# Kernel tuning notes

Hardware: AMD Instinct MI355X
Metric: run time of the kernel (lower is better)

## Reference

```python
import jax, jax.numpy as jnp
import numpy as np

B, N, C = 16, 65536, 21          # batch, anchors, classes (class 0 = background)
TH_CONF = 0.05                   # confidence threshold
TH_IOU = 0.5                     # NMS IoU threshold
TOP_K = 200                      # candidates kept per (batch, class) before NMS
V0, V1 = 0.1, 0.2                # SSD box-coder variances


def setup_inputs() -> dict:
    key = jax.random.key(0)
    k1, k2, k3, k4 = jax.random.split(key, 4)
    conf = jax.random.normal(k1, (B, N, C), dtype=jnp.float32)
    loc = jax.random.normal(k2, (B, N, 4), dtype=jnp.float32)
    # anchors in center form (cx, cy, w, h), normalized coords
    cxcy = jax.random.uniform(k3, (N, 2), dtype=jnp.float32)
    wh = 0.02 + 0.2 * jax.random.uniform(k4, (N, 2), dtype=jnp.float32)
    anchors = jnp.concatenate([cxcy, wh], axis=-1)
    return {"conf": conf, "loc": loc, "anchors": anchors}


def _decode(anchors, loc):
    # SSD decode: anchors [N,4] center form, loc [B,N,4] offsets -> [B,N,4] xyxy
    a_xy, a_wh = anchors[:, :2], anchors[:, 2:]
    xy = a_xy + loc[..., :2] * V0 * a_wh
    wh = a_wh * jnp.exp(loc[..., 2:] * V1)
    return jnp.concatenate([xy - 0.5 * wh, xy + 0.5 * wh], axis=-1)


def _iou(boxes):
    # boxes [K,4] xyxy -> pairwise IoU [K,K]
    area = jnp.maximum(boxes[:, 2] - boxes[:, 0], 0.0) * jnp.maximum(boxes[:, 3] - boxes[:, 1], 0.0)
    lt = jnp.maximum(boxes[:, None, :2], boxes[None, :, :2])
    rb = jnp.minimum(boxes[:, None, 2:], boxes[None, :, 2:])
    wh = jnp.maximum(rb - lt, 0.0)
    inter = wh[..., 0] * wh[..., 1]
    union = area[:, None] + area[None, :] - inter
    return inter / jnp.maximum(union, 1e-9)


def _nms_keep(iou, valid):
    # greedy NMS over score-sorted candidates; valid = (score >= TH_CONF)
    K = iou.shape[0]
    idx = jnp.arange(K)

    def body(keep, xs):
        row, v, i = xs
        suppressed = jnp.any((row > TH_IOU) & keep & (idx < i))
        k = v & (~suppressed)
        return keep.at[i].set(k), 0

    keep, _ = jax.lax.scan(body, jnp.zeros((K,), dtype=bool), (iou, valid, idx))
    return keep


def reference(conf, loc, anchors):
    score = jax.nn.softmax(conf, axis=2)            # [B,N,C]
    boxes = _decode(anchors, loc)                   # [B,N,4]
    # skip background class 0 (cls_base = 1 for softmax classifier)
    cls_scores = jnp.swapaxes(score[..., 1:], 1, 2)  # [B,C-1,N]
    top_s, top_i = jax.lax.top_k(cls_scores, TOP_K)  # [B,C-1,K], sorted desc
    top_boxes = jax.vmap(lambda bx, ix: bx[ix])(boxes, top_i)  # [B,C-1,K,4]
    valid = top_s >= TH_CONF
    keep = jax.vmap(jax.vmap(lambda b, v: _nms_keep(_iou(b), v)))(top_boxes, valid)  # [B,C-1,K]
    out_boxes = jnp.where(keep[..., None], top_boxes, 0.0)
    out_scores = jnp.where(keep, top_s, 0.0)
    return jnp.concatenate([out_boxes, out_scores[..., None]], axis=-1)  # [B,C-1,K,5]
```

## Files before the change

kernel.cpp:

```cpp
#include <hip/hip_runtime.h>
#include <stdint.h>

#define NB     16
#define NANCH  65536
#define NC     21
#define NCLS   20
#define NCOL   (NB * NCLS)
#define TOPK   200
#define NBINS  1024
#define CAP    256
#define CAPCOL 4096
#define CAPFAST 2048
#define CNTSTRIDE 16

constexpr float TH      = 0.05f;
constexpr float TPRE    = 0.20f;
constexpr float SCALE20 = (float)NBINS / 0.80f;
constexpr float SCALE05 = (float)NBINS / 0.95f;

__device__ __forceinline__ int bin20(float s) {
  int b = (int)((s - 0.20f) * SCALE20);
  return b < 0 ? 0 : (b > NBINS - 1 ? NBINS - 1 : b);
}
__device__ __forceinline__ int bin05(float s) {
  int b = (int)((s - 0.05f) * SCALE05);
  return b < 0 ? 0 : (b > NBINS - 1 ? NBINS - 1 : b);
}

__device__ __forceinline__ unsigned long long rl64(unsigned long long v, int lane) {
  unsigned int lo = __builtin_amdgcn_readlane((int)(unsigned int)v, lane);
  unsigned int hi = __builtin_amdgcn_readlane((int)(unsigned int)(v >> 32), lane);
  return ((unsigned long long)hi << 32) | lo;
}

__device__ __forceinline__ void softmax_tail(const float* x, float* e, float& S) {
  float m = x[0];
#pragma unroll
  for (int c = 1; c < NC; ++c) m = fmaxf(m, x[c]);
#pragma unroll
  for (int c = 0; c < NC; ++c) e[c] = expf(x[c] - m);
  float r0 = e[0] + e[8],  r1 = e[1] + e[9],  r2 = e[2] + e[10], r3 = e[3] + e[11];
  float r4 = e[4] + e[12], r5 = e[5] + e[13], r6 = e[6] + e[14], r7 = e[7] + e[15];
  S = ((r0 + r1) + (r2 + r3)) + ((r4 + r5) + (r6 + r7));
  S += e[16]; S += e[17]; S += e[18]; S += e[19]; S += e[20];
}

__global__ __launch_bounds__(256) void softmax_collect_kernel(
    const float* __restrict__ conf,
    unsigned int* __restrict__ cnt, unsigned long long* __restrict__ cand) {
  const int tid = threadIdx.x;
  __shared__ float ld[256 * NC];
  const float4* src = (const float4*)conf + (long long)blockIdx.x * 1344;
  float4* dst4 = (float4*)ld;
#pragma unroll
  for (int i = 0; i < 5; ++i) dst4[tid + i * 256] = src[tid + i * 256];
  if (tid < 64) dst4[tid + 1280] = src[tid + 1280];
  __syncthreads();

  const int a = blockIdx.x * 256 + tid;
  const int b = a >> 16;
  const int n = a & (NANCH - 1);
  float x[NC];
#pragma unroll
  for (int c = 0; c < NC; ++c) x[c] = ld[tid * NC + c];
  float e[NC], S;
  softmax_tail(x, e, S);
  const float t = TPRE * S;
  unsigned int takemask = 0;
#pragma unroll
  for (int c = 0; c < NCLS; ++c)
    if (e[c + 1] >= t) takemask |= (1u << c);

  __shared__ unsigned int wcnt[4][NCLS];
  __shared__ unsigned int wbase[4][NCLS];
  const int wave = tid >> 6, lane = tid & 63;
#pragma unroll
  for (int c = 0; c < NCLS; ++c) {
    unsigned long long m = __ballot((takemask >> c) & 1);
    if (lane == 0) wcnt[wave][c] = (unsigned int)__popcll(m);
  }
  __syncthreads();
  if (tid < NCLS) {
    const int c = tid;
    unsigned int t0 = wcnt[0][c], t1 = wcnt[1][c], t2 = wcnt[2][c], t3 = wcnt[3][c];
    unsigned int tot = t0 + t1 + t2 + t3;
    unsigned int base = tot ? atomicAdd(&cnt[(b * NCLS + c) * CNTSTRIDE], tot) : 0u;
    wbase[0][c] = base;
    wbase[1][c] = base + t0;
    wbase[2][c] = base + t0 + t1;
    wbase[3][c] = base + t0 + t1 + t2;
  }
  __syncthreads();
#pragma unroll
  for (int c = 0; c < NCLS; ++c) {
    bool take = (takemask >> c) & 1;
    unsigned long long m = __ballot(take);
    if (take) {
      float s = e[c + 1] / S;
      unsigned int off = wbase[wave][c] +
                         (unsigned int)__popcll(m & ((1ULL << lane) - 1));
      if (off < CAPCOL) {
        unsigned int key = __float_as_uint(s) | 0x80000000u;
        cand[(long long)(b * NCLS + c) * CAPCOL + off] =
            ((unsigned long long)(key ^ 0xFFFFFFFFu) << 32) |
            (unsigned long long)(unsigned int)n;
      }
    }
  }
}

__global__ __launch_bounds__(1024) void topk_nms_kernel(
    const unsigned long long* __restrict__ candg,
    const unsigned int* __restrict__ cnt,
    const float* __restrict__ conf, const float* __restrict__ loc,
    const float* __restrict__ anchors, float* __restrict__ out) {
  const int bc = blockIdx.x;
  const int b  = bc / NCLS;
  const int cls = bc % NCLS;
  const int tid = threadIdx.x;
  const int lane = tid & 63;

  __shared__ unsigned int hist[NBINS];
  __shared__ unsigned int part[256];
  __shared__ int s_sel, s_n;
  __shared__ unsigned long long cand[CAP];
  __shared__ float4 box4[TOPK];
  __shared__ float sscore[TOPK];
  __shared__ unsigned long long adj[TOPK][4];
  __shared__ unsigned long long keptw[4];

  int nc = (int)cnt[bc * CNTSTRIDE];
  const bool fast = (nc >= TOPK && nc <= CAPFAST);
  for (int i = tid; i < NBINS; i += 1024) hist[i] = 0;
  if (tid < CAP) cand[tid] = ~0ULL;
  if (tid < TOPK) { box4[tid] = make_float4(0.f,0.f,0.f,0.f); sscore[tid] = 0.f; }
  if (tid == 0) s_n = 0;
  __syncthreads();

  const unsigned long long* cg = candg + (long long)bc * CAPCOL;
  if (fast) {
    for (int i = tid; i < nc; i += 1024) {
      unsigned int key = (unsigned int)(cg[i] >> 32) ^ 0xFFFFFFFFu;
      float s = __uint_as_float(key ^ 0x80000000u);
      atomicAdd(&hist[bin20(s)], 1u);
    }
  } else {
    for (int n = tid; n < NANCH; n += 1024) {
      const float* row = conf + ((long long)b * NANCH + n) * NC;
      float x[NC], e[NC], S;
#pragma unroll
      for (int c = 0; c < NC; ++c) x[c] = row[c];
      softmax_tail(x, e, S);
      float s = e[cls + 1] / S;
      if (s >= TH) atomicAdd(&hist[bin05(s)], 1u);
    }
  }
  __syncthreads();

  if (tid < 256)
    part[tid] = hist[tid*4] + hist[tid*4+1] + hist[tid*4+2] + hist[tid*4+3];
  if (tid == 0) s_sel = -1;
  __syncthreads();
  if (tid < 64) {
    unsigned int p4 = part[tid*4] + part[tid*4+1] + part[tid*4+2] + part[tid*4+3];
    unsigned int sfx = p4;
#pragma unroll
    for (int off = 1; off < 64; off <<= 1) {
      unsigned int o = __shfl_down(sfx, off);
      if (tid + off < 64) sfx += o;
    }
    unsigned int above = sfx - p4;
    if (above < TOPK && sfx >= TOPK) {
      unsigned int cum = above; int sel = tid * 16; bool found = false;
      for (int q = 3; q >= 0 && !found; --q) {
        unsigned int pc = part[tid*4 + q];
        if (cum + pc >= TOPK) {
          for (int i = 3; i >= 0; --i) {
            unsigned int c = hist[(tid*4+q)*4 + i];
            if (cum + c >= TOPK) { sel = (tid*4+q)*4 + i; found = true; break; }
            cum += c;
          }
        } else cum += pc;
      }
      s_sel = sel;
    }
  }
  __syncthreads();
  const int sel = s_sel;

  if (fast) {
    const int ncr = (nc + 1023) & ~1023;
    for (int i = tid; i < ncr; i += 1024) {
      bool have = i < nc;
      unsigned long long k64 = have ? cg[i] : 0ULL;
      bool takeit = false;
      if (have) {
        unsigned int key = (unsigned int)(k64 >> 32) ^ 0xFFFFFFFFu;
        float s = __uint_as_float(key ^ 0x80000000u);
        takeit = bin20(s) >= sel;
      }
      unsigned long long m = __ballot(takeit);
      int cw = (int)__popcll(m);
      int base = 0;
      if (lane == 0 && cw) base = atomicAdd(&s_n, cw);
      base = __shfl(base, 0);
      if (takeit) {
        int pos = base + (int)__popcll(m & ((1ULL << lane) - 1));
        if (pos < CAP) cand[pos] = k64;
      }
    }
  } else {
    for (int n0 = tid; n0 < NANCH; n0 += 1024) {
      const float* row = conf + ((long long)b * NANCH + n0) * NC;
      float x[NC], e[NC], S;
#pragma unroll
      for (int c = 0; c < NC; ++c) x[c] = row[c];
      softmax_tail(x, e, S);
      float s = e[cls + 1] / S;
      bool takeit = (s >= TH && (sel < 0 || bin05(s) >= sel));
      unsigned long long m = __ballot(takeit);
      int cw = (int)__popcll(m);
      int base = 0;
      if (lane == 0 && cw) base = atomicAdd(&s_n, cw);
      base = __shfl(base, 0);
      if (takeit) {
        int pos = base + (int)__popcll(m & ((1ULL << lane) - 1));
        if (pos < CAP) {
          unsigned int key = __float_as_uint(s) | 0x80000000u;
          cand[pos] = ((unsigned long long)(key ^ 0xFFFFFFFFu) << 32) |
                      (unsigned long long)(unsigned int)n0;
        }
      }
    }
  }
  __syncthreads();
  int ncand = s_n; if (ncand > CAP) ncand = CAP;
  const int nsel = (ncand < TOPK) ? ncand : TOPK;

  if (tid < CAP && tid < ncand) {
    const unsigned long long key64 = cand[tid];
    int rank = 0;
#pragma unroll 8
    for (int j = 0; j < CAP; ++j)
      rank += (cand[j] < key64) ? 1 : 0;
    if (rank < TOPK) {
      unsigned int key = (unsigned int)(key64 >> 32) ^ 0xFFFFFFFFu;
      float s = __uint_as_float(key ^ 0x80000000u);
      int idx = (int)(unsigned int)(key64 & 0xFFFFFFFFu);
      float4 anc = ((const float4*)anchors)[idx];
      float4 l   = ((const float4*)loc)[(long long)b * NANCH + idx];
      float cx = anc.x + (l.x * 0.1f) * anc.z;
      float cy = anc.y + (l.y * 0.1f) * anc.w;
      float w  = anc.z * expf(l.z * 0.2f);
      float h  = anc.w * expf(l.w * 0.2f);
      box4[rank] = make_float4(cx - 0.5f * w, cy - 0.5f * h,
                               cx + 0.5f * w, cy + 0.5f * h);
      sscore[rank] = s;
    }
  }
  __syncthreads();

  if (tid < TOPK * 4) {
    const int row = tid >> 2, w = tid & 3;
    const float4 a4 = box4[row];
    const float aar = fmaxf(a4.z - a4.x, 0.f) * fmaxf(a4.w - a4.y, 0.f);
    const int jend = (w < 3) ? 64 : (TOPK - 192);
    unsigned long long roww = 0;
#pragma unroll 4
    for (int jj = 0; jj < jend; ++jj) {
      const int j = (w << 6) + jj;
      float4 b4 = box4[j];
      float jar = fmaxf(b4.z - b4.x, 0.f) * fmaxf(b4.w - b4.y, 0.f);
      float ltx = fmaxf(a4.x, b4.x);
      float lty = fmaxf(a4.y, b4.y);
      float rbx = fminf(a4.z, b4.z);
      float rby = fminf(a4.w, b4.w);
      float iw = fmaxf(rbx - ltx, 0.0f);
      float ih = fmaxf(rby - lty, 0.0f);
      float inter = iw * ih;
      float uni = aar + jar - inter;
      float um = fmaxf(uni, 1e-9f);
      float half = 0.5f * um;
      bool hit;
      if (inter > half * 1.000001f)      hit = true;
      else if (inter < half * 0.999999f) hit = false;
      else                               hit = (inter / um > 0.5f);
      roww |= (unsigned long long)(hit ? 1u : 0u) << jj;
    }
    const int myw = row >> 6, myb = row & 63;
    unsigned long long tri = (w < myw) ? 0ULL
                           : (w > myw) ? ~0ULL
                           : ((myb == 63) ? 0ULL : (~0ULL << (myb + 1)));
    adj[row][w] = roww & tri;
  }
  __syncthreads();

  if (tid < 64) {
    const int l = tid;
    unsigned long long r0[4], r1[4], r2[4], r3[4];
#pragma unroll
    for (int w = 0; w < 4; ++w) {
      r0[w] = adj[l][w];
      r1[w] = adj[l + 64][w];
      r2[w] = adj[l + 128][w];
      r3[w] = (l < 8) ? adj[l + 192][w] : 0ULL;
    }
    unsigned long long sup0 = 0, sup1 = 0, sup2 = 0, sup3 = 0;
    unsigned long long k0 = 0, k1 = 0, k2 = 0, k3 = 0;
#pragma unroll 1
    for (int ii = 0; ii < 64; ++ii) {
      unsigned long long live = ((~sup0 >> ii) & 1ULL) &
                                (unsigned long long)(ii < nsel);
      unsigned long long mask = 0ULL - live;
      k0 |= live << ii;
      sup0 |= rl64(r0[0], ii) & mask; sup1 |= rl64(r0[1], ii) & mask;
      sup2 |= rl64(r0[2], ii) & mask; sup3 |= rl64(r0[3], ii) & mask;
    }
#pragma unroll 1
    for (int ii = 0; ii < 64; ++ii) {
      unsigned long long live = ((~sup1 >> ii) & 1ULL) &
                                (unsigned long long)((64 + ii) < nsel);
      unsigned long long mask = 0ULL - live;
      k1 |= live << ii;
      sup1 |= rl64(r1[1], ii) & mask; sup2 |= rl64(r1[2], ii) & mask;
      sup3 |= rl64(r1[3], ii) & mask;
    }
#pragma unroll 1
    for (int ii = 0; ii < 64; ++ii) {
      unsigned long long live = ((~sup2 >> ii) & 1ULL) &
                                (unsigned long long)((128 + ii) < nsel);
      unsigned long long mask = 0ULL - live;
      k2 |= live << ii;
      sup2 |= rl64(r2[2], ii) & mask; sup3 |= rl64(r2[3], ii) & mask;
    }
#pragma unroll 1
    for (int ii = 0; ii < 8; ++ii) {
      unsigned long long live = ((~sup3 >> ii) & 1ULL) &
                                (unsigned long long)((192 + ii) < nsel);
      unsigned long long mask = 0ULL - live;
      k3 |= live << ii;
      sup3 |= rl64(r3[3], ii) & mask;
    }
    if (l == 0) { keptw[0] = k0; keptw[1] = k1; keptw[2] = k2; keptw[3] = k3; }
  }
  __syncthreads();

  const float* fb = (const float*)box4;
  float* ob = out + (long long)bc * (TOPK * 5);
  for (int pos = tid; pos < TOPK * 5; pos += 1024) {
    int row = pos / 5;
    int k5  = pos - row * 5;
    bool kp = (keptw[row >> 6] >> (row & 63)) & 1ULL;
    float val = (k5 == 4) ? sscore[row] : fb[row * 4 + k5];
    ob[pos] = kp ? val : 0.0f;
  }
}

extern "C" void kernel_launch(void* const* d_in, const int* in_sizes, int n_in,
                              void* d_out, int out_size, void* d_ws, size_t ws_size,
                              hipStream_t stream) {
  const float* conf    = (const float*)d_in[0];
  const float* loc     = (const float*)d_in[1];
  const float* anchors = (const float*)d_in[2];
  float* out = (float*)d_out;

  char* ws = (char*)d_ws;
  unsigned long long* cand = (unsigned long long*)ws;
  unsigned int*       cnt  = (unsigned int*)(ws + 10485760);

  hipMemsetAsync(ws + 10485760, 0, 320 * CNTSTRIDE * 4, stream);
  softmax_collect_kernel<<<(NB * NANCH) / 256, 256, 0, stream>>>(conf, cnt, cand);
  topk_nms_kernel<<<NCOL, 1024, 0, stream>>>(cand, cnt, conf, loc, anchors, out);
}
```

Before: 94.14 us.

## Process two (batch,class) columns per block in top-k NMS kernel

The top-k/NMS kernel now handles two columns per 1024-thread block, so it launches half as many blocks. Histogram, selection, ranking, IoU and greedy-NMS phases run both columns side by side, which raises thread utilisation in the phases that previously used only 64-800 threads. The cost is doubled shared memory per block, which may lower occupancy. With 320 columns the grid drops to 160 blocks, fewer than the number of CUs on the device, so parallelism across CUs falls.

```diff
diff --git a/kernel.cpp b/kernel.cpp
--- a/kernel.cpp
+++ b/kernel.cpp
@@ -114,162 +114,194 @@
     const unsigned int* __restrict__ cnt,
     const float* __restrict__ conf, const float* __restrict__ loc,
     const float* __restrict__ anchors, float* __restrict__ out) {
-  const int bc = blockIdx.x;
-  const int b  = bc / NCLS;
-  const int cls = bc % NCLS;
+  const int bc0 = blockIdx.x * 2;
   const int tid = threadIdx.x;
   const int lane = tid & 63;
 
-  __shared__ unsigned int hist[NBINS];
-  __shared__ unsigned int part[256];
-  __shared__ int s_sel, s_n;
-  __shared__ unsigned long long cand[CAP];
-  __shared__ float4 box4[TOPK];
-  __shared__ float sscore[TOPK];
-  __shared__ unsigned long long adj[TOPK][4];
-  __shared__ unsigned long long keptw[4];
-
-  int nc = (int)cnt[bc * CNTSTRIDE];
-  const bool fast = (nc >= TOPK && nc <= CAPFAST);
-  for (int i = tid; i < NBINS; i += 1024) hist[i] = 0;
-  if (tid < CAP) cand[tid] = ~0ULL;
-  if (tid < TOPK) { box4[tid] = make_float4(0.f,0.f,0.f,0.f); sscore[tid] = 0.f; }
-  if (tid == 0) s_n = 0;
-  __syncthreads();
-
-  const unsigned long long* cg = candg + (long long)bc * CAPCOL;
-  if (fast) {
-    for (int i = tid; i < nc; i += 1024) {
-      unsigned int key = (unsigned int)(cg[i] >> 32) ^ 0xFFFFFFFFu;
-      float s = __uint_as_float(key ^ 0x80000000u);
-      atomicAdd(&hist[bin20(s)], 1u);
-    }
-  } else {
-    for (int n = tid; n < NANCH; n += 1024) {
-      const float* row = conf + ((long long)b * NANCH + n) * NC;
-      float x[NC], e[NC], S;
-#pragma unroll
-      for (int c = 0; c < NC; ++c) x[c] = row[c];
-      softmax_tail(x, e, S);
-      float s = e[cls + 1] / S;
-      if (s >= TH) atomicAdd(&hist[bin05(s)], 1u);
-    }
-  }
-  __syncthreads();
-
-  if (tid < 256)
-    part[tid] = hist[tid*4] + hist[tid*4+1] + hist[tid*4+2] + hist[tid*4+3];
-  if (tid == 0) s_sel = -1;
-  __syncthreads();
-  if (tid < 64) {
-    unsigned int p4 = part[tid*4] + part[tid*4+1] + part[tid*4+2] + part[tid*4+3];
+  __shared__ unsigned int hist[2][NBINS];
+  __shared__ unsigned int part[2][256];
+  __shared__ int s_sel[2], s_n[2];
+  __shared__ unsigned long long cand[2][CAP];
+  __shared__ float4 box4[2][TOPK];
+  __shared__ float sscore[2][TOPK];
+  __shared__ unsigned long long adj[2][TOPK][4];
+  __shared__ unsigned long long keptw[2][4];
+
+  const int nc0 = (int)cnt[bc0 * CNTSTRIDE];
+  const int nc1 = (int)cnt[(bc0 + 1) * CNTSTRIDE];
+  const bool fast0 = (nc0 >= TOPK && nc0 <= CAPFAST);
+  const bool fast1 = (nc1 >= TOPK && nc1 <= CAPFAST);
+
+  for (int i = tid; i < 2 * NBINS; i += 1024) ((unsigned int*)hist)[i] = 0;
+  if (tid < 2 * CAP) ((unsigned long long*)cand)[tid] = ~0ULL;
+  if (tid < 2 * TOPK) {
+    ((float4*)box4)[tid] = make_float4(0.f, 0.f, 0.f, 0.f);
+    ((float*)sscore)[tid] = 0.f;
+  }
+  if (tid < 2) s_n[tid] = 0;
+  __syncthreads();
+
+#pragma unroll
+  for (int c = 0; c < 2; ++c) {
+    const int ncc = c ? nc1 : nc0;
+    const bool fc = c ? fast1 : fast0;
+    const int bcc = bc0 + c;
+    if (fc) {
+      const unsigned long long* cg = candg + (long long)bcc * CAPCOL;
+      for (int i = tid; i < ncc; i += 1024) {
+        unsigned int key = (unsigned int)(cg[i] >> 32) ^ 0xFFFFFFFFu;
+        float s = __uint_as_float(key ^ 0x80000000u);
+        atomicAdd(&hist[c][bin20(s)], 1u);
+      }
+    } else {
+      const int bb = bcc / NCLS, cls = bcc % NCLS;
+      for (int n = tid; n < NANCH; n += 1024) {
+        const float* row = conf + ((long long)bb * NANCH + n) * NC;
+        float x[NC], e[NC], S;
+#pragma unroll
+        for (int cc = 0; cc < NC; ++cc) x[cc] = row[cc];
+        softmax_tail(x, e, S);
+        float s = e[cls + 1] / S;
+        if (s >= TH) atomicAdd(&hist[c][bin05(s)], 1u);
+      }
+    }
+  }
+  __syncthreads();
+
+  if (tid < 512) {
+    const int c = tid >> 8, t = tid & 255;
+    part[c][t] = hist[c][t*4] + hist[c][t*4+1] + hist[c][t*4+2] + hist[c][t*4+3];
+  }
+  if (tid < 2) s_sel[tid] = -1;
+  __syncthreads();
+  if (tid < 128) {
+    const int c = tid >> 6, l = tid & 63;
+    unsigned int p4 = part[c][l*4] + part[c][l*4+1] +
+                      part[c][l*4+2] + part[c][l*4+3];
     unsigned int sfx = p4;
 #pragma unroll
     for (int off = 1; off < 64; off <<= 1) {
       unsigned int o = __shfl_down(sfx, off);
-      if (tid + off < 64) sfx += o;
+      if (l + off < 64) sfx += o;
     }
     unsigned int above = sfx - p4;
     if (above < TOPK && sfx >= TOPK) {
-      unsigned int cum = above; int sel = tid * 16; bool found = false;
+      unsigned int cum = above; int sel = l * 16; bool found = false;
       for (int q = 3; q >= 0 && !found; --q) {
-        unsigned int pc = part[tid*4 + q];
+        unsigned int pc = part[c][l*4 + q];
         if (cum + pc >= TOPK) {
           for (int i = 3; i >= 0; --i) {
-            unsigned int c = hist[(tid*4+q)*4 + i];
-            if (cum + c >= TOPK) { sel = (tid*4+q)*4 + i; found = true; break; }
-            cum += c;
+            unsigned int cc = hist[c][(l*4+q)*4 + i];
+            if (cum + cc >= TOPK) { sel = (l*4+q)*4 + i; found = true; break; }
+            cum += cc;
           }
         } else cum += pc;
       }
-      s_sel = sel;
-    }
-  }
-  __syncthreads();
-  const int sel = s_sel;
-
-  if (fast) {
-    const int ncr = (nc + 1023) & ~1023;
-    for (int i = tid; i < ncr; i += 1024) {
-      bool have = i < nc;
-      unsigned long long k64 = have ? cg[i] : 0ULL;
-      bool takeit = false;
-      if (have) {
-        unsigned int key = (unsigned int)(k64 >> 32) ^ 0xFFFFFFFFu;
+      s_sel[c] = sel;
+    }
+  }
+  __syncthreads();
+
+#pragma unroll
+  for (int c = 0; c < 2; ++c) {
+    const int ncc = c ? nc1 : nc0;
+    const bool fc = c ? fast1 : fast0;
+    const int bcc = bc0 + c;
+    const int sel = s_sel[c];
+    if (fc) {
+      const unsigned long long* cg = candg + (long long)bcc * CAPCOL;
+      const int ncr = (ncc + 1023) & ~1023;
+      for (int i = tid; i < ncr; i += 1024) {
+        bool have = i < ncc;
+        unsigned long long k64 = have ? cg[i] : 0ULL;
+        bool takeit = false;
+        if (have) {
+          unsigned int key = (unsigned int)(k64 >> 32) ^ 0xFFFFFFFFu;
+          float s = __uint_as_float(key ^ 0x80000000u);
+          takeit = bin20(s) >= sel;
+        }
+        unsigned long long m = __ballot(takeit);
+        int cw = (int)__popcll(m);
+        int base = 0;
+        if (lane == 0 && cw) base = atomicAdd(&s_n[c], cw);
+        base = __shfl(base, 0);
+        if (takeit) {
+          int pos = base + (int)__popcll(m & ((1ULL << lane) - 1));
+          if (pos < CAP) cand[c][pos] = k64;
+        }
+      }
+    } else {
+      const int bb = bcc / NCLS, cls = bcc % NCLS;
+      for (int n0 = tid; n0 < NANCH; n0 += 1024) {
+        const float* row = conf + ((long long)bb * NANCH + n0) * NC;
+        float x[NC], e[NC], S;
+#pragma unroll
+        for (int cc = 0; cc < NC; ++cc) x[cc] = row[cc];
+        softmax_tail(x, e, S);
+        float s = e[cls + 1] / S;
+        bool takeit = (s >= TH && (sel < 0 || bin05(s) >= sel));
+        unsigned long long m = __ballot(takeit);
+        int cw = (int)__popcll(m);
+        int base = 0;
+        if (lane == 0 && cw) base = atomicAdd(&s_n[c], cw);
+        base = __shfl(base, 0);
+        if (takeit) {
+          int pos = base + (int)__popcll(m & ((1ULL << lane) - 1));
+          if (pos < CAP) {
+            unsigned int key = __float_as_uint(s) | 0x80000000u;
+            cand[c][pos] = ((unsigned long long)(key ^ 0xFFFFFFFFu) << 32) |
+                           (unsigned long long)(unsigned int)n0;
+          }
+        }
+      }
+    }
+  }
+  __syncthreads();
+  int ncand0 = s_n[0]; if (ncand0 > CAP) ncand0 = CAP;
+  int ncand1 = s_n[1]; if (ncand1 > CAP) ncand1 = CAP;
+  const int nsel0 = (ncand0 < TOPK) ? ncand0 : TOPK;
+  const int nsel1 = (ncand1 < TOPK) ? ncand1 : TOPK;
+
+  if (tid < 512) {
+    const int c = tid >> 8, t = tid & 255;
+    const int ncand = c ? ncand1 : ncand0;
+    const int bcc = bc0 + c;
+    const int bb = bcc / NCLS;
+    if (t < ncand) {
+      const unsigned long long key64 = cand[c][t];
+      int rank = 0;
+#pragma unroll 8
+      for (int j = 0; j < CAP; ++j)
+        rank += (cand[c][j] < key64) ? 1 : 0;
+      if (rank < TOPK) {
+        unsigned int key = (unsigned int)(key64 >> 32) ^ 0xFFFFFFFFu;
         float s = __uint_as_float(key ^ 0x80000000u);
-        takeit = bin20(s) >= sel;
-      }
-      unsigned long long m = __ballot(takeit);
-      int cw = (int)__popcll(m);
-      int base = 0;
-      if (lane == 0 && cw) base = atomicAdd(&s_n, cw);
-      base = __shfl(base, 0);
-      if (takeit) {
-        int pos = base + (int)__popcll(m & ((1ULL << lane) - 1));
-        if (pos < CAP) cand[pos] = k64;
-      }
-    }
-  } else {
-    for (int n0 = tid; n0 < NANCH; n0 += 1024) {
-      const float* row = conf + ((long long)b * NANCH + n0) * NC;
-      float x[NC], e[NC], S;
-#pragma unroll
-      for (int c = 0; c < NC; ++c) x[c] = row[c];
-      softmax_tail(x, e, S);
-      float s = e[cls + 1] / S;
-      bool takeit = (s >= TH && (sel < 0 || bin05(s) >= sel));
-      unsigned long long m = __ballot(takeit);
-      int cw = (int)__popcll(m);
-      int base = 0;
-      if (lane == 0 && cw) base = atomicAdd(&s_n, cw);
-      base = __shfl(base, 0);
-      if (takeit) {
-        int pos = base + (int)__popcll(m & ((1ULL << lane) - 1));
-        if (pos < CAP) {
-          unsigned int key = __float_as_uint(s) | 0x80000000u;
-          cand[pos] = ((unsigned long long)(key ^ 0xFFFFFFFFu) << 32) |
-                      (unsigned long long)(unsigned int)n0;
-        }
-      }
-    }
-  }
-  __syncthreads();
-  int ncand = s_n; if (ncand > CAP) ncand = CAP;
-  const int nsel = (ncand < TOPK) ? ncand : TOPK;
-
-  if (tid < CAP && tid < ncand) {
-    const unsigned long long key64 = cand[tid];
-    int rank = 0;
-#pragma unroll 8
-    for (int j = 0; j < CAP; ++j)
-      rank += (cand[j] < key64) ? 1 : 0;
-    if (rank < TOPK) {
-      unsigned int key = (unsigned int)(key64 >> 32) ^ 0xFFFFFFFFu;
-      float s = __uint_as_float(key ^ 0x80000000u);
-      int idx = (int)(unsigned int)(key64 & 0xFFFFFFFFu);
-      float4 anc = ((const float4*)anchors)[idx];
-      float4 l   = ((const float4*)loc)[(long long)b * NANCH + idx];
-      float cx = anc.x + (l.x * 0.1f) * anc.z;
-      float cy = anc.y + (l.y * 0.1f) * anc.w;
-      float w  = anc.z * expf(l.z * 0.2f);
-      float h  = anc.w * expf(l.w * 0.2f);
-      box4[rank] = make_float4(cx - 0.5f * w, cy - 0.5f * h,
-                               cx + 0.5f * w, cy + 0.5f * h);
-      sscore[rank] = s;
-    }
-  }
-  __syncthreads();
-
-  if (tid < TOPK * 4) {
-    const int row = tid >> 2, w = tid & 3;
-    const float4 a4 = box4[row];
+        int idx = (int)(unsigned int)(key64 & 0xFFFFFFFFu);
+        float4 anc = ((const float4*)anchors)[idx];
+        float4 l   = ((const float4*)loc)[(long long)bb * NANCH + idx];
+        float cx = anc.x + (l.x * 0.1f) * anc.z;
+        float cy = anc.y + (l.y * 0.1f) * anc.w;
+        float w  = anc.z * expf(l.z * 0.2f);
+        float h  = anc.w * expf(l.w * 0.2f);
+        box4[c][rank] = make_float4(cx - 0.5f * w, cy - 0.5f * h,
+                                    cx + 0.5f * w, cy + 0.5f * h);
+        sscore[c][rank] = s;
+      }
+    }
+  }
+  __syncthreads();
+
+  for (int T = tid; T < 2 * TOPK * 4; T += 1024) {
+    const int c = T & 1, rw = T >> 1;
+    const int row = rw >> 2, w = rw & 3;
+    const float4 a4 = box4[c][row];
     const float aar = fmaxf(a4.z - a4.x, 0.f) * fmaxf(a4.w - a4.y, 0.f);
     const int jend = (w < 3) ? 64 : (TOPK - 192);
     unsigned long long roww = 0;
 #pragma unroll 4
     for (int jj = 0; jj < jend; ++jj) {
       const int j = (w << 6) + jj;
-      float4 b4 = box4[j];
+      float4 b4 = box4[c][j];
       float jar = fmaxf(b4.z - b4.x, 0.f) * fmaxf(b4.w - b4.y, 0.f);
       float ltx = fmaxf(a4.x, b4.x);
       float lty = fmaxf(a4.y, b4.y);
@@ -291,19 +323,20 @@
     unsigned long long tri = (w < myw) ? 0ULL
                            : (w > myw) ? ~0ULL
                            : ((myb == 63) ? 0ULL : (~0ULL << (myb + 1)));
-    adj[row][w] = roww & tri;
-  }
-  __syncthreads();
-
-  if (tid < 64) {
-    const int l = tid;
+    adj[c][row][w] = roww & tri;
+  }
+  __syncthreads();
+
+  if (tid < 128) {
+    const int c = tid >> 6, l = tid & 63;
+    const int nsel = c ? nsel1 : nsel0;
     unsigned long long r0[4], r1[4], r2[4], r3[4];
 #pragma unroll
     for (int w = 0; w < 4; ++w) {
-      r0[w] = adj[l][w];
-      r1[w] = adj[l + 64][w];
-      r2[w] = adj[l + 128][w];
-      r3[w] = (l < 8) ? adj[l + 192][w] : 0ULL;
+      r0[w] = adj[c][l][w];
+      r1[w] = adj[c][l + 64][w];
+      r2[w] = adj[c][l + 128][w];
+      r3[w] = (l < 8) ? adj[c][l + 192][w] : 0ULL;
     }
     unsigned long long sup0 = 0, sup1 = 0, sup2 = 0, sup3 = 0;
     unsigned long long k0 = 0, k1 = 0, k2 = 0, k3 = 0;
@@ -341,18 +374,22 @@
       k3 |= live << ii;
       sup3 |= rl64(r3[3], ii) & mask;
     }
-    if (l == 0) { keptw[0] = k0; keptw[1] = k1; keptw[2] = k2; keptw[3] = k3; }
-  }
-  __syncthreads();
-
-  const float* fb = (const float*)box4;
-  float* ob = out + (long long)bc * (TOPK * 5);
-  for (int pos = tid; pos < TOPK * 5; pos += 1024) {
-    int row = pos / 5;
-    int k5  = pos - row * 5;
-    bool kp = (keptw[row >> 6] >> (row & 63)) & 1ULL;
-    float val = (k5 == 4) ? sscore[row] : fb[row * 4 + k5];
-    ob[pos] = kp ? val : 0.0f;
+    if (l == 0) { keptw[c][0] = k0; keptw[c][1] = k1;
+                  keptw[c][2] = k2; keptw[c][3] = k3; }
+  }
+  __syncthreads();
+
+#pragma unroll
+  for (int c = 0; c < 2; ++c) {
+    const float* fb = (const float*)box4[c];
+    float* ob = out + (long long)(bc0 + c) * (TOPK * 5);
+    for (int pos = tid; pos < TOPK * 5; pos += 1024) {
+      int row = pos / 5;
+      int k5  = pos - row * 5;
+      bool kp = (keptw[c][row >> 6] >> (row & 63)) & 1ULL;
+      float val = (k5 == 4) ? sscore[c][row] : fb[row * 4 + k5];
+      ob[pos] = kp ? val : 0.0f;
+    }
   }
 }
 
@@ -370,5 +407,6 @@
 
   hipMemsetAsync(ws + 10485760, 0, 320 * CNTSTRIDE * 4, stream);
   softmax_collect_kernel<<<(NB * NANCH) / 256, 256, 0, stream>>>(conf, cnt, cand);
-  topk_nms_kernel<<<NCOL, 1024, 0, stream>>>(cand, cnt, conf, loc, anchors, out);
-}
+  topk_nms_kernel<<<NCOL / 2, 1024, 0, stream>>>(cand, cnt, conf, loc, anchors,
+                                                 out);
+}
```

After: 93.31 us. Within noise of the previous version (-0.9%).
